# Performance work log

Hardware: AMD Instinct MI355X
Metric: run time of the kernel (lower is better)

## Reference

```python
import jax, jax.numpy as jnp
import numpy as np

B, S, D, H = 4, 2048, 1024, 16
DK = D // H

def setup_inputs() -> dict:
    key = jax.random.key(0)
    ks = jax.random.split(key, 5)
    scale = 1.0 / np.sqrt(D)
    return {
        "x": jax.random.normal(ks[0], (B, S, D), dtype=jnp.float32),
        "Wq": jax.random.normal(ks[1], (H, D, DK), dtype=jnp.float32) * scale,
        "Wk": jax.random.normal(ks[2], (H, D, DK), dtype=jnp.float32) * scale,
        "Wv": jax.random.normal(ks[3], (H, D, DK), dtype=jnp.float32) * scale,
        "Wo": jax.random.normal(ks[4], (D, D), dtype=jnp.float32) * scale,
    }

def reference(x, Wq, Wk, Wv, Wo):
    # x: [B,S,D]; Wq/Wk/Wv: [H,D,DK] (stacked per-head Linear weights); Wo: [D,D]
    seq = x.shape[-2]
    q = jnp.einsum('bsd,hdk->bhsk', x, Wq)
    k = jnp.einsum('bsd,hdk->bhsk', x, Wk)
    v = jnp.einsum('bsd,hdk->bhsk', x, Wv)
    dk = q.shape[-1]
    scores = jnp.einsum('bhqk,bhsk->bhqs', q, k) / jnp.sqrt(jnp.asarray(dk, x.dtype))
    # causal mask: mask out strictly-future positions (triu, diagonal=1)
    causal = jnp.tril(jnp.ones((seq, seq), dtype=bool))  # True = keep
    scores = jnp.where(causal, scores, -jnp.inf)
    probs = jax.nn.softmax(scores, axis=-1)  # attn_pdrop = 0.0 -> dropout is identity
    attn = jnp.einsum('bhqs,bhsk->bhqk', probs, v)
    # concat heads: [B,S,H*DK]
    concat = attn.transpose(0, 2, 1, 3).reshape(x.shape[0], seq, -1)
    # output_proj: nn.Linear(D, D, bias=False) -> y = concat @ Wo.T
    return jnp.einsum('bsd,ed->bse', concat, Wo)
```

## Files before the change

kernel.cpp:

```cpp
#include <hip/hip_runtime.h>
#include <hip/hip_bf16.h>

#define B_ 4
#define S_ 2048
#define D_ 1024
#define H_ 16
#define DK_ 64

typedef __attribute__((ext_vector_type(8))) short bf16x8;
typedef __attribute__((ext_vector_type(4))) float f32x4;
typedef __attribute__((ext_vector_type(4))) unsigned int u32x4;

__device__ __forceinline__ unsigned short f2bf(float f) {
    unsigned int u = __float_as_uint(f);
    u += 0x7FFFu + ((u >> 16) & 1u);
    return (unsigned short)(u >> 16);
}

__device__ __forceinline__ unsigned int cvtpk_bf16(float lo, float hi) {
    unsigned int r;
    asm("v_cvt_pk_bf16_f32 %0, %1, %2" : "=v"(r) : "v"(lo), "v"(hi));
    return r;
}

__global__ void cvt_kernel(const float* __restrict__ src, unsigned short* __restrict__ dst) {
    int i = (blockIdx.x * 256 + threadIdx.x) * 8;
    float4 f0 = *(const float4*)&src[i];
    float4 f1 = *(const float4*)&src[i + 4];
    unsigned short t[8] __attribute__((aligned(16))) = {
        f2bf(f0.x), f2bf(f0.y), f2bf(f0.z), f2bf(f0.w),
        f2bf(f1.x), f2bf(f1.y), f2bf(f1.z), f2bf(f1.w)};
    *(u32x4*)&dst[i] = *(const u32x4*)t;
}

__global__ void prepack_kernel(const float* __restrict__ Wq,
                               const float* __restrict__ Wk,
                               const float* __restrict__ Wv,
                               unsigned short* __restrict__ Wt) {
    __shared__ unsigned short Ts[64 * 65];
    int h = blockIdx.x, w3 = blockIdx.y, t = blockIdx.z;
    const float* src = (w3 == 0 ? Wq : (w3 == 1 ? Wk : Wv)) + h * D_ * DK_ + t * 64 * DK_;
    unsigned short* dst = Wt + (w3 * H_ + h) * DK_ * D_ + t * 64;
    const float wscale = (w3 == 0) ? 0.18033688011112042f : 1.0f;
    int tid = threadIdx.x;
    for (int rep = 0; rep < 16; ++rep) {
        int idx = rep * 256 + tid;
        int dl = idx >> 6, k = idx & 63;
        Ts[k * 65 + dl] = f2bf(src[dl * 64 + k] * wscale);
    }
    __syncthreads();
    for (int rep = 0; rep < 16; ++rep) {
        int idx = rep * 256 + tid;
        int kl = idx >> 6, dl = idx & 63;
        dst[kl * D_ + dl] = Ts[kl * 65 + dl];
    }
}

__device__ __forceinline__ void stage128_async(const unsigned short* __restrict__ g,
                                               unsigned short* lds_base, int wv, int lane, int ldg) {
#pragma unroll
    for (int it = 0; it < 4; ++it) {
        int rbase = wv * 32 + it * 8;
        int r = rbase + (lane >> 3);
        int gc = (lane & 7) ^ ((lane >> 3) & 7);
        const unsigned short* gp = g + r * ldg + gc * 8;
        unsigned short* lp = lds_base + rbase * 64;
        __builtin_amdgcn_global_load_lds((const __attribute__((address_space(1))) unsigned int*)gp,
                                         (__attribute__((address_space(3))) unsigned int*)lp,
                                         16, 0, 0);
    }
}

__device__ __forceinline__ void stage64_async(const unsigned short* __restrict__ g,
                                              unsigned short* lds_base, int wv, int lane, int ldg) {
#pragma unroll
    for (int it = 0; it < 2; ++it) {
        int rbase = wv * 16 + it * 8;
        int r = rbase + (lane >> 3);
        int gc = (lane & 7) ^ ((lane >> 3) & 7);
        const unsigned short* gp = g + r * ldg + gc * 8;
        unsigned short* lp = lds_base + rbase * 64;
        __builtin_amdgcn_global_load_lds((const __attribute__((address_space(1))) unsigned int*)gp,
                                         (__attribute__((address_space(3))) unsigned int*)lp,
                                         16, 0, 0);
    }
}

template <bool QKV_OUT>
__global__ __launch_bounds__(256) void gemm128_kernel(const unsigned short* __restrict__ A,
                                                      const unsigned short* __restrict__ Bt,
                                                      void* __restrict__ Out,
                                                      unsigned short* __restrict__ VtOut) {
    __shared__ __align__(16) unsigned short smem[2 * 128 * 64];
    unsigned short* As = smem;
    unsigned short* Bs = smem + 128 * 64;
    const int tid = threadIdx.x;
    const int wv = tid >> 6, lane = tid & 63, l15 = lane & 15, q4 = lane >> 4;
    const int wm = wv >> 1, wn = wv & 1;
    const int r0 = blockIdx.x * 128, c0 = blockIdx.y * 128;

    const unsigned short* Ab = A + r0 * D_;
    const unsigned short* Bb = Bt + c0 * D_;

    f32x4 acc[4][4] = {};

    for (int kt = 0; kt < 16; ++kt) {
        stage128_async(Ab + kt * 64, As, wv, lane, D_);
        stage128_async(Bb + kt * 64, Bs, wv, lane, D_);
        __syncthreads();
#pragma unroll
        for (int kk = 0; kk < 2; ++kk) {
            bf16x8 af[4], bf[4];
            const int sw = ((kk * 4 + q4) ^ (l15 & 7)) * 8;
#pragma unroll
            for (int i = 0; i < 4; ++i) {
                af[i] = *(const bf16x8*)&As[(wm * 64 + i * 16 + l15) * 64 + sw];
                bf[i] = *(const bf16x8*)&Bs[(wn * 64 + i * 16 + l15) * 64 + sw];
            }
#pragma unroll
            for (int i = 0; i < 4; ++i)
#pragma unroll
                for (int j = 0; j < 4; ++j)
                    acc[i][j] = __builtin_amdgcn_mfma_f32_16x16x32_bf16(af[i], bf[j], acc[i][j], 0, 0, 0);
        }
        __syncthreads();
    }

    if (QKV_OUT && c0 >= 2 * D_) {
        const int b = r0 >> 11, s0 = r0 & (S_ - 1);
#pragma unroll
        for (int i = 0; i < 4; ++i)
#pragma unroll
            for (int j = 0; j < 4; ++j)
#pragma unroll
                for (int rr = 0; rr < 4; ++rr) {
                    int col = wn * 64 + j * 16 + l15;
                    int row = wm * 64 + i * 16 + q4 * 4 + rr;
                    smem[col * 128 + (row ^ ((col & 7) * 8))] = f2bf(acc[i][j][rr]);
                }
        __syncthreads();
#pragma unroll
        for (int rep = 0; rep < 8; ++rep) {
            int idx = rep * 256 + tid;
            int col = idx >> 4, ch = idx & 15;
            u32x4 v = *(const u32x4*)&smem[col * 128 + ((ch * 8) ^ ((col & 7) * 8))];
            int gcol = c0 + col;
            int vrow = b * 1024 + (gcol & 1023);
            *(u32x4*)&VtOut[vrow * S_ + s0 + ch * 8] = v;
        }
    } else {
#pragma unroll
        for (int i = 0; i < 4; ++i)
#pragma unroll
            for (int j = 0; j < 4; ++j)
#pragma unroll
                for (int rr = 0; rr < 4; ++rr) {
                    int grow = r0 + wm * 64 + i * 16 + q4 * 4 + rr;
                    int gcol = c0 + wn * 64 + j * 16 + l15;
                    if (QKV_OUT) {
                        int b = grow >> 11, s = grow & (S_ - 1);
                        int w3 = gcol >> 10, h = (gcol >> 6) & 15, dk = gcol & 63;
                        ((unsigned short*)Out)[(((w3 * B_ + b) * H_ + h) * S_ + s) * DK_ + dk] =
                            f2bf(acc[i][j][rr]);
                    } else {
                        ((float*)Out)[grow * D_ + gcol] = acc[i][j][rr];
                    }
                }
    }
}

__global__ __launch_bounds__(256) void attn_kernel(const unsigned short* __restrict__ qkv,
                                                   unsigned short* __restrict__ concat) {
    static const int J[16] = {15, 13, 11, 9, 0, 2, 4, 6, 14, 12, 10, 8, 1, 3, 5, 7};
    const int bh = blockIdx.x;
    const int b = bh >> 4, h = bh & 15;
    const int j = J[blockIdx.y];
    const int q0 = j * 128;
    const int nk = 2 * j + 2;

    const unsigned short* Qp = qkv + ((0 * B_ + b) * H_ + h) * S_ * DK_;
    const unsigned short* Kp = qkv + ((1 * B_ + b) * H_ + h) * S_ * DK_;
    const unsigned short* Vt = qkv + 2 * B_ * H_ * S_ * DK_ + (b * H_ + h) * DK_ * S_;

    __shared__ __align__(16) unsigned short Kb[2][64 * 64];
    __shared__ __align__(16) unsigned short Vb[2][64 * 64];

    const int tid = threadIdx.x;
    const int wv = tid >> 6, lane = tid & 63, l15 = lane & 15, q4 = lane >> 4;

    stage64_async(Kp, Kb[0], wv, lane, DK_);
    stage64_async(Vt, Vb[0], wv, lane, S_);

    bf16x8 aq[2][2];
#pragma unroll
    for (int rt = 0; rt < 2; ++rt)
#pragma unroll
        for (int kk = 0; kk < 2; ++kk)
            aq[rt][kk] = *(const bf16x8*)&Qp[(q0 + wv * 32 + rt * 16 + l15) * DK_ + kk * 32 + q4 * 8];

    f32x4 o[2][4] = {};
    float l_[2] = {0.0f, 0.0f};

    __syncthreads();

    for (int t = 0; t < nk; ++t) {
        const int k0 = t * 64;
        if (t + 1 < nk) {
            stage64_async(Kp + (k0 + 64) * DK_, Kb[(t + 1) & 1], wv, lane, DK_);
            stage64_async(Vt + (k0 + 64), Vb[(t + 1) & 1], wv, lane, S_);
        }
        const unsigned short* Kt = Kb[t & 1];
        const unsigned short* Vtt = Vb[t & 1];

        if ((t + 1 < nk) || (wv >= 2)) {
            f32x4 sa[2][4] = {};
            __builtin_amdgcn_s_setprio(1);
#pragma unroll
            for (int kk = 0; kk < 2; ++kk) {
                const int sw = ((kk * 4 + q4) ^ (l15 & 7)) * 8;
#pragma unroll
                for (int ct = 0; ct < 4; ++ct) {
                    bf16x8 bk = *(const bf16x8*)&Kt[(ct * 16 + l15) * 64 + sw];
                    sa[0][ct] = __builtin_amdgcn_mfma_f32_16x16x32_bf16(bk, aq[0][kk], sa[0][ct], 0, 0, 0);
                    sa[1][ct] = __builtin_amdgcn_mfma_f32_16x16x32_bf16(bk, aq[1][kk], sa[1][ct], 0, 0, 0);
                }
            }
            __builtin_amdgcn_s_setprio(0);

            if (t < nk - 2) {
#pragma unroll
                for (int rt = 0; rt < 2; ++rt)
#pragma unroll
                    for (int ct = 0; ct < 4; ++ct)
#pragma unroll
                        for (int r = 0; r < 4; ++r)
                            sa[rt][ct][r] = __builtin_amdgcn_exp2f(sa[rt][ct][r]);
            } else {
                const int kb = k0 + q4 * 4;
#pragma unroll
                for (int rt = 0; rt < 2; ++rt) {
                    const int qrow = q0 + wv * 32 + rt * 16 + l15;
#pragma unroll
                    for (int ct = 0; ct < 4; ++ct)
#pragma unroll
                        for (int r = 0; r < 4; ++r) {
                            float e = __builtin_amdgcn_exp2f(sa[rt][ct][r]);
                            sa[rt][ct][r] = (kb + ct * 16 + r <= qrow) ? e : 0.0f;
                        }
                }
            }

#pragma unroll
            for (int rt = 0; rt < 2; ++rt)
#pragma unroll
                for (int ct = 0; ct < 4; ++ct)
                    l_[rt] += (sa[rt][ct][0] + sa[rt][ct][1]) + (sa[rt][ct][2] + sa[rt][ct][3]);

            bf16x8 F[2][2];
#pragma unroll
            for (int rt = 0; rt < 2; ++rt)
#pragma unroll
                for (int kk = 0; kk < 2; ++kk) {
                    u32x4 w;
#pragma unroll
                    for (int u = 0; u < 2; ++u) {
                        unsigned int a = cvtpk_bf16(sa[rt][2 * kk][2 * u], sa[rt][2 * kk][2 * u + 1]);
                        unsigned int c = cvtpk_bf16(sa[rt][2 * kk + 1][2 * u], sa[rt][2 * kk + 1][2 * u + 1]);
                        asm("v_permlane32_swap_b32 %0, %1" : "+v"(a), "+v"(c));
                        asm("v_permlane16_swap_b32 %0, %1" : "+v"(a), "+v"(c));
                        w[u] = a;
                        w[2 + u] = c;
                    }
                    F[rt][kk] = *(const bf16x8*)&w;
                }

            __builtin_amdgcn_s_setprio(1);
#pragma unroll
            for (int kk = 0; kk < 2; ++kk) {
                const int sw = ((kk * 4 + q4) ^ (l15 & 7)) * 8;
#pragma unroll
                for (int cd = 0; cd < 4; ++cd) {
                    bf16x8 bv = *(const bf16x8*)&Vtt[(cd * 16 + l15) * 64 + sw];
                    o[0][cd] = __builtin_amdgcn_mfma_f32_16x16x32_bf16(F[0][kk], bv, o[0][cd], 0, 0, 0);
                    o[1][cd] = __builtin_amdgcn_mfma_f32_16x16x32_bf16(F[1][kk], bv, o[1][cd], 0, 0, 0);
                }
            }
            __builtin_amdgcn_s_setprio(0);
        }
        __syncthreads();
    }

#pragma unroll
    for (int rt = 0; rt < 2; ++rt) {
        float lr = l_[rt];
        lr += __shfl_xor(lr, 16);
        lr += __shfl_xor(lr, 32);
#pragma unroll
        for (int r = 0; r < 4; ++r) {
            float lfull = __shfl(lr, (lane & 48) | (q4 * 4 + r));
            float inv = 1.0f / fmaxf(lfull, 1.0e-37f);
            int row = q0 + wv * 32 + rt * 16 + q4 * 4 + r;
#pragma unroll
            for (int cd = 0; cd < 4; ++cd) {
                int col = h * DK_ + cd * 16 + l15;
                concat[(b * S_ + row) * D_ + col] = f2bf(o[rt][cd][r] * inv);
            }
        }
    }
}

extern "C" void kernel_launch(void* const* d_in, const int* in_sizes, int n_in,
                              void* d_out, int out_size, void* d_ws, size_t ws_size,
                              hipStream_t stream) {
    const float* x  = (const float*)d_in[0];
    const float* Wq = (const float*)d_in[1];
    const float* Wk = (const float*)d_in[2];
    const float* Wv = (const float*)d_in[3];
    const float* Wo = (const float*)d_in[4];

    unsigned short* qkv    = (unsigned short*)d_ws;
    unsigned short* Wt     = qkv + 3 * B_ * H_ * S_ * DK_;
    unsigned short* xbf    = Wt + 3 * H_ * DK_ * D_;
    unsigned short* concat = xbf;
    unsigned short* Wobf   = Wt;
    unsigned short* VtOut  = qkv + 2 * B_ * H_ * S_ * DK_;

    cvt_kernel<<<B_ * S_ * D_ / 2048, 256, 0, stream>>>(x, xbf);
    prepack_kernel<<<dim3(H_, 3, 16), 256, 0, stream>>>(Wq, Wk, Wv, Wt);
    gemm128_kernel<true><<<dim3(B_ * S_ / 128, 3 * H_ * DK_ / 128), 256, 0, stream>>>(xbf, Wt, qkv, VtOut);
    cvt_kernel<<<D_ * D_ / 2048, 256, 0, stream>>>(Wo, Wobf);
    attn_kernel<<<dim3(64, 16), 256, 0, stream>>>(qkv, concat);
    gemm128_kernel<false><<<dim3(B_ * S_ / 128, D_ / 128), 256, 0, stream>>>(concat, Wobf, d_out, nullptr);
}
```

Before: 250.4 us.

## Replace 128x128 GEMM with 128x256 double-buffered 8-wave pipelined GEMM

Replaces the projection GEMM with a 512-thread kernel that computes 128x256 tiles. It double-buffers A and B halves in LDS and interleaves async global-to-LDS loads with four MFMA phases, using explicit vmcnt waits and barriers in place of full syncthreads. It also swizzles the block order for L2 locality and raises MFMA priority with setprio. This aims to overlap memory with compute and cut the barrier stalls of the single-buffered loop, at the cost of more LDS per block, fewer blocks, and hand-tuned wait counts that must stay correct.

```diff
diff --git a/kernel.cpp b/kernel.cpp
--- a/kernel.cpp
+++ b/kernel.cpp
@@ -22,6 +22,8 @@
     asm("v_cvt_pk_bf16_f32 %0, %1, %2" : "=v"(r) : "v"(lo), "v"(hi));
     return r;
 }
+
+#define BAR() do { __builtin_amdgcn_s_barrier(); asm volatile("" ::: "memory"); } while (0)
 
 __global__ void cvt_kernel(const float* __restrict__ src, unsigned short* __restrict__ dst) {
     int i = (blockIdx.x * 256 + threadIdx.x) * 8;
@@ -56,18 +58,27 @@
     }
 }
 
-__device__ __forceinline__ void stage128_async(const unsigned short* __restrict__ g,
-                                               unsigned short* lds_base, int wv, int lane, int ldg) {
-#pragma unroll
-    for (int it = 0; it < 4; ++it) {
-        int rbase = wv * 32 + it * 8;
+__device__ __forceinline__ void gload16(const unsigned short* gp, unsigned short* lp) {
+    __builtin_amdgcn_global_load_lds((const __attribute__((address_space(1))) unsigned int*)gp,
+                                     (__attribute__((address_space(3))) unsigned int*)lp,
+                                     16, 0, 0);
+}
+
+__device__ __forceinline__ void stageA_half(const unsigned short* __restrict__ g,
+                                            unsigned short* lds_base, int wv, int lane, int ldg) {
+    int r = wv * 8 + (lane >> 3);
+    int gc = (lane & 7) ^ ((lane >> 3) & 7);
+    gload16(g + r * ldg + gc * 8, lds_base + (wv * 8) * 64);
+}
+
+__device__ __forceinline__ void stageB_half(const unsigned short* __restrict__ g,
+                                            unsigned short* lds_base, int wv, int lane, int ldg) {
+#pragma unroll
+    for (int L = 0; L < 2; ++L) {
+        int rbase = wv * 16 + L * 8;
         int r = rbase + (lane >> 3);
         int gc = (lane & 7) ^ ((lane >> 3) & 7);
-        const unsigned short* gp = g + r * ldg + gc * 8;
-        unsigned short* lp = lds_base + rbase * 64;
-        __builtin_amdgcn_global_load_lds((const __attribute__((address_space(1))) unsigned int*)gp,
-                                         (__attribute__((address_space(3))) unsigned int*)lp,
-                                         16, 0, 0);
+        gload16(g + r * ldg + gc * 8, lds_base + rbase * 64);
     }
 }
 
@@ -78,94 +89,150 @@
         int rbase = wv * 16 + it * 8;
         int r = rbase + (lane >> 3);
         int gc = (lane & 7) ^ ((lane >> 3) & 7);
-        const unsigned short* gp = g + r * ldg + gc * 8;
-        unsigned short* lp = lds_base + rbase * 64;
-        __builtin_amdgcn_global_load_lds((const __attribute__((address_space(1))) unsigned int*)gp,
-                                         (__attribute__((address_space(3))) unsigned int*)lp,
-                                         16, 0, 0);
-    }
+        gload16(g + r * ldg + gc * 8, lds_base + rbase * 64);
+    }
+}
+
+template <int MH, int NH>
+__device__ __forceinline__ void phase_mfma(const unsigned short* Asl, const unsigned short* Bsl,
+                                           int db, int wm, int wn, int l15, int q4,
+                                           f32x4 (&acc)[2][2][2][2]) {
+    bf16x8 af[2][2], bf[2][2];
+#pragma unroll
+    for (int kk = 0; kk < 2; ++kk) {
+        const int sw = ((kk * 4 + q4) ^ (l15 & 7)) * 8;
+#pragma unroll
+        for (int m4 = 0; m4 < 2; ++m4)
+            af[m4][kk] = *(const bf16x8*)&Asl[(db + MH) * 4096 + (wm * 32 + m4 * 16 + l15) * 64 + sw];
+#pragma unroll
+        for (int n2 = 0; n2 < 2; ++n2)
+            bf[n2][kk] = *(const bf16x8*)&Bsl[(db + NH) * 8192 + (wn * 32 + n2 * 16 + l15) * 64 + sw];
+    }
+    __builtin_amdgcn_s_setprio(1);
+#pragma unroll
+    for (int kk = 0; kk < 2; ++kk)
+#pragma unroll
+        for (int m4 = 0; m4 < 2; ++m4)
+#pragma unroll
+            for (int n2 = 0; n2 < 2; ++n2)
+                acc[MH][NH][m4][n2] =
+                    __builtin_amdgcn_mfma_f32_16x16x32_bf16(af[m4][kk], bf[n2][kk], acc[MH][NH][m4][n2], 0, 0, 0);
+    __builtin_amdgcn_s_setprio(0);
 }
 
 template <bool QKV_OUT>
-__global__ __launch_bounds__(256) void gemm128_kernel(const unsigned short* __restrict__ A,
+__global__ __launch_bounds__(512) void gemm256_kernel(const unsigned short* __restrict__ A,
                                                       const unsigned short* __restrict__ Bt,
                                                       void* __restrict__ Out,
                                                       unsigned short* __restrict__ VtOut) {
-    __shared__ __align__(16) unsigned short smem[2 * 128 * 64];
-    unsigned short* As = smem;
-    unsigned short* Bs = smem + 128 * 64;
+    __shared__ __align__(16) unsigned short lds[49152];
+    unsigned short* Asl = lds;
+    unsigned short* Bsl = lds + 16384;
+
     const int tid = threadIdx.x;
     const int wv = tid >> 6, lane = tid & 63, l15 = lane & 15, q4 = lane >> 4;
-    const int wm = wv >> 1, wn = wv & 1;
-    const int r0 = blockIdx.x * 128, c0 = blockIdx.y * 128;
+    const int wm = wv >> 2, wn = wv & 3;
+
+    const int nwg = gridDim.x * gridDim.y;
+    const int bid = blockIdx.x + blockIdx.y * gridDim.x;
+    const int swz = (bid & 7) * (nwg >> 3) + (bid >> 3);
+    const int bx = swz % gridDim.x, by = swz / gridDim.x;
+    const int r0 = bx * 128, c0 = by * 256;
 
     const unsigned short* Ab = A + r0 * D_;
     const unsigned short* Bb = Bt + c0 * D_;
 
-    f32x4 acc[4][4] = {};
-
-    for (int kt = 0; kt < 16; ++kt) {
-        stage128_async(Ab + kt * 64, As, wv, lane, D_);
-        stage128_async(Bb + kt * 64, Bs, wv, lane, D_);
-        __syncthreads();
-#pragma unroll
-        for (int kk = 0; kk < 2; ++kk) {
-            bf16x8 af[4], bf[4];
-            const int sw = ((kk * 4 + q4) ^ (l15 & 7)) * 8;
-#pragma unroll
-            for (int i = 0; i < 4; ++i) {
-                af[i] = *(const bf16x8*)&As[(wm * 64 + i * 16 + l15) * 64 + sw];
-                bf[i] = *(const bf16x8*)&Bs[(wn * 64 + i * 16 + l15) * 64 + sw];
-            }
-#pragma unroll
-            for (int i = 0; i < 4; ++i)
-#pragma unroll
-                for (int j = 0; j < 4; ++j)
-                    acc[i][j] = __builtin_amdgcn_mfma_f32_16x16x32_bf16(af[i], bf[j], acc[i][j], 0, 0, 0);
-        }
-        __syncthreads();
-    }
+    f32x4 acc[2][2][2][2] = {};
+
+    stageA_half(Ab, Asl, wv, lane, D_);
+    stageB_half(Bb, Bsl, wv, lane, D_);
+    stageB_half(Bb + 128 * D_, Bsl + 8192, wv, lane, D_);
+
+    for (int j = 0; j < 16; ++j) {
+        const int db = (j & 1) * 2;
+        const int ndb = ((j + 1) & 1) * 2;
+        const bool nx = (j + 1 < 16);
+
+        stageA_half(Ab + 64 * D_ + j * 64, Asl + (db + 1) * 4096, wv, lane, D_);
+        asm volatile("s_waitcnt vmcnt(3)" ::: "memory");
+        BAR();
+        phase_mfma<0, 0>(Asl, Bsl, db, wm, wn, l15, q4, acc);
+
+        if (nx) {
+            stageA_half(Ab + (j + 1) * 64, Asl + (ndb + 0) * 4096, wv, lane, D_);
+            asm volatile("s_waitcnt vmcnt(2)" ::: "memory");
+        } else {
+            asm volatile("s_waitcnt vmcnt(1)" ::: "memory");
+        }
+        BAR();
+        phase_mfma<0, 1>(Asl, Bsl, db, wm, wn, l15, q4, acc);
+
+        if (nx) {
+            stageB_half(Bb + (j + 1) * 64, Bsl + (ndb + 0) * 8192, wv, lane, D_);
+            asm volatile("s_waitcnt vmcnt(3)" ::: "memory");
+        } else {
+            asm volatile("s_waitcnt vmcnt(0)" ::: "memory");
+        }
+        BAR();
+        phase_mfma<1, 1>(Asl, Bsl, db, wm, wn, l15, q4, acc);
+
+        if (nx) stageB_half(Bb + 128 * D_ + (j + 1) * 64, Bsl + (ndb + 1) * 8192, wv, lane, D_);
+        BAR();
+        phase_mfma<1, 0>(Asl, Bsl, db, wm, wn, l15, q4, acc);
+    }
+
+    __syncthreads();
 
     if (QKV_OUT && c0 >= 2 * D_) {
         const int b = r0 >> 11, s0 = r0 & (S_ - 1);
 #pragma unroll
-        for (int i = 0; i < 4; ++i)
-#pragma unroll
-            for (int j = 0; j < 4; ++j)
-#pragma unroll
-                for (int rr = 0; rr < 4; ++rr) {
-                    int col = wn * 64 + j * 16 + l15;
-                    int row = wm * 64 + i * 16 + q4 * 4 + rr;
-                    smem[col * 128 + (row ^ ((col & 7) * 8))] = f2bf(acc[i][j][rr]);
-                }
-        __syncthreads();
-#pragma unroll
-        for (int rep = 0; rep < 8; ++rep) {
-            int idx = rep * 256 + tid;
-            int col = idx >> 4, ch = idx & 15;
-            u32x4 v = *(const u32x4*)&smem[col * 128 + ((ch * 8) ^ ((col & 7) * 8))];
-            int gcol = c0 + col;
-            int vrow = b * 1024 + (gcol & 1023);
-            *(u32x4*)&VtOut[vrow * S_ + s0 + ch * 8] = v;
+        for (int nh = 0; nh < 2; ++nh) {
+#pragma unroll
+            for (int mh = 0; mh < 2; ++mh)
+#pragma unroll
+                for (int m4 = 0; m4 < 2; ++m4)
+#pragma unroll
+                    for (int n2 = 0; n2 < 2; ++n2)
+#pragma unroll
+                        for (int rr = 0; rr < 4; ++rr) {
+                            int cl = wn * 32 + n2 * 16 + l15;
+                            int rl = mh * 64 + wm * 32 + m4 * 16 + q4 * 4 + rr;
+                            lds[cl * 128 + (rl ^ ((cl & 7) * 8))] = f2bf(acc[mh][nh][m4][n2][rr]);
+                        }
+            __syncthreads();
+#pragma unroll
+            for (int rep = 0; rep < 4; ++rep) {
+                int idx = rep * 512 + tid;
+                int col = idx >> 4, ch = idx & 15;
+                u32x4 v = *(const u32x4*)&lds[col * 128 + ((ch * 8) ^ ((col & 7) * 8))];
+                int gcol = c0 + nh * 128 + col;
+                int vrow = b * 1024 + (gcol & 1023);
+                *(u32x4*)&VtOut[vrow * S_ + s0 + ch * 8] = v;
+            }
+            __syncthreads();
         }
     } else {
 #pragma unroll
-        for (int i = 0; i < 4; ++i)
-#pragma unroll
-            for (int j = 0; j < 4; ++j)
-#pragma unroll
-                for (int rr = 0; rr < 4; ++rr) {
-                    int grow = r0 + wm * 64 + i * 16 + q4 * 4 + rr;
-                    int gcol = c0 + wn * 64 + j * 16 + l15;
-                    if (QKV_OUT) {
-                        int b = grow >> 11, s = grow & (S_ - 1);
-                        int w3 = gcol >> 10, h = (gcol >> 6) & 15, dk = gcol & 63;
-                        ((unsigned short*)Out)[(((w3 * B_ + b) * H_ + h) * S_ + s) * DK_ + dk] =
-                            f2bf(acc[i][j][rr]);
-                    } else {
-                        ((float*)Out)[grow * D_ + gcol] = acc[i][j][rr];
-                    }
-                }
+        for (int mh = 0; mh < 2; ++mh)
+#pragma unroll
+            for (int nh = 0; nh < 2; ++nh)
+#pragma unroll
+                for (int m4 = 0; m4 < 2; ++m4)
+#pragma unroll
+                    for (int n2 = 0; n2 < 2; ++n2)
+#pragma unroll
+                        for (int rr = 0; rr < 4; ++rr) {
+                            int grow = r0 + mh * 64 + wm * 32 + m4 * 16 + q4 * 4 + rr;
+                            int gcol = c0 + nh * 128 + wn * 32 + n2 * 16 + l15;
+                            if (QKV_OUT) {
+                                int b = grow >> 11, s = grow & (S_ - 1);
+                                int w3 = gcol >> 10, h = (gcol >> 6) & 15, dk = gcol & 63;
+                                ((unsigned short*)Out)[(((w3 * B_ + b) * H_ + h) * S_ + s) * DK_ + dk] =
+                                    f2bf(acc[mh][nh][m4][n2][rr]);
+                            } else {
+                                ((float*)Out)[grow * D_ + gcol] = acc[mh][nh][m4][n2][rr];
+                            }
+                        }
     }
 }
 
@@ -327,8 +394,8 @@
 
     cvt_kernel<<<B_ * S_ * D_ / 2048, 256, 0, stream>>>(x, xbf);
     prepack_kernel<<<dim3(H_, 3, 16), 256, 0, stream>>>(Wq, Wk, Wv, Wt);
-    gemm128_kernel<true><<<dim3(B_ * S_ / 128, 3 * H_ * DK_ / 128), 256, 0, stream>>>(xbf, Wt, qkv, VtOut);
+    gemm256_kernel<true><<<dim3(64, 12), 512, 0, stream>>>(xbf, Wt, qkv, VtOut);
     cvt_kernel<<<D_ * D_ / 2048, 256, 0, stream>>>(Wo, Wobf);
     attn_kernel<<<dim3(64, 16), 256, 0, stream>>>(qkv, concat);
-    gemm128_kernel<false><<<dim3(B_ * S_ / 128, D_ / 128), 256, 0, stream>>>(concat, Wobf, d_out, nullptr);
-}
+    gemm256_kernel<false><<<dim3(64, 4), 512, 0, stream>>>(concat, Wobf, d_out, nullptr);
+}
```

After: 247.3 us. No clear change (-1.2%).
